# Optimization experiments

Measured on AMD Instinct MI355X. Metric: run time of the kernel, lower is better.

Reference implementation:

```python
import jax, jax.numpy as jnp
import numpy as np

T, H, I, E, TOPK = 4096, 2048, 2048, 16, 2

def setup_inputs() -> dict:
    key = jax.random.key(0)
    k1, k2, k3, k4 = jax.random.split(key, 4)
    return {
        "x": jax.random.normal(k1, (T, H), dtype=jnp.float32),
        "gate_w": jax.random.normal(k2, (E, H), dtype=jnp.float32) * 0.02,
        "ws": jax.random.normal(k3, (E, 2 * I, H), dtype=jnp.float32) * 0.02,
        "w2s": jax.random.normal(k4, (E, H, I), dtype=jnp.float32) * 0.02,
        "top_k": TOPK,
    }

def reference(x, gate_w, ws, w2s, top_k):
    # Router: logits -> softmax -> topk -> renormalize (top_k > 1), per fused_topk.
    logits = x @ gate_w.T                      # [T, E]
    scores = jax.nn.softmax(logits, axis=-1)
    topk_w, topk_ids = jax.lax.top_k(scores, top_k)  # [T, K]
    if top_k > 1:
        topk_w = topk_w / jnp.sum(topk_w, axis=-1, keepdims=True)
    n_exp, two_i, _ = ws.shape
    i_dim = two_i // 2

    def expert_step(acc, inp):
        w13_e, w2_e, e = inp               # [2I,H], [H,I], scalar
        gate_up = x @ w13_e.T              # [T, 2I]
        g, u = gate_up[:, :i_dim], gate_up[:, i_dim:]
        h = jax.nn.silu(g) * u             # SiluAndMul
        y = h @ w2_e.T                     # [T, H]
        coef = jnp.sum(jnp.where(topk_ids == e, topk_w, 0.0), axis=-1)  # [T]
        return acc + coef[:, None] * y, None

    init = jnp.zeros_like(x)
    eids = jnp.arange(n_exp, dtype=topk_ids.dtype)
    out, _ = jax.lax.scan(expert_step, init, (ws, w2s, eids))
    return out
```

## Files before the change

kernel.cpp:

```cpp
#include <hip/hip_runtime.h>
#include <hip/hip_bf16.h>

#define T_DIM 4096
#define H_DIM 2048
#define I_DIM 2048
#define E_NUM 16

#define BM 128
#define BN 128
#define BK 32

#define MAX_ROWS 10240

using frag_ab = __attribute__((ext_vector_type(8))) short;
using frag_cd = __attribute__((ext_vector_type(4))) float;

__device__ __forceinline__ unsigned short f2bf(float f) {
    unsigned int u = __float_as_uint(f);
    u += 0x7fff + ((u >> 16) & 1);
    return (unsigned short)(u >> 16);
}
__device__ __forceinline__ float bf2f(unsigned short s) {
    return __uint_as_float(((unsigned int)s) << 16);
}

__global__ void routing_kernel(const float* __restrict__ x,
                               const float* __restrict__ gw,
                               int* __restrict__ cnt,
                               int* __restrict__ tok_list,
                               float* __restrict__ tok_w) {
    const int wave = threadIdx.x >> 6;
    const int lane = threadIdx.x & 63;
    const int t = blockIdx.x * 4 + wave;
    if (t >= T_DIM) return;

    float acc[E_NUM];
#pragma unroll
    for (int e = 0; e < E_NUM; ++e) acc[e] = 0.f;
    const float* xr = x + (size_t)t * H_DIM;
    for (int j = lane; j < H_DIM; j += 64) {
        float xv = xr[j];
#pragma unroll
        for (int e = 0; e < E_NUM; ++e)
            acc[e] = fmaf(xv, gw[e * H_DIM + j], acc[e]);
    }
#pragma unroll
    for (int e = 0; e < E_NUM; ++e) {
        float v = acc[e];
#pragma unroll
        for (int off = 32; off > 0; off >>= 1) v += __shfl_xor(v, off);
        acc[e] = v;
    }
    if (lane == 0) {
        int b1 = 0; float l1 = acc[0];
#pragma unroll
        for (int e = 1; e < E_NUM; ++e)
            if (acc[e] > l1) { l1 = acc[e]; b1 = e; }
        int b2 = -1; float l2 = -1e30f;
#pragma unroll
        for (int e = 0; e < E_NUM; ++e)
            if (e != b1 && acc[e] > l2) { l2 = acc[e]; b2 = e; }
        float w1 = 1.f / (1.f + __expf(l2 - l1));
        float w2 = 1.f - w1;
        int p1 = atomicAdd(&cnt[b1], 1);
        tok_list[b1 * T_DIM + p1] = t; tok_w[b1 * T_DIM + p1] = w1;
        int p2 = atomicAdd(&cnt[b2], 1);
        tok_list[b2 * T_DIM + p2] = t; tok_w[b2 * T_DIM + p2] = w2;
    }
}

__global__ void scan_kernel(const int* __restrict__ cnt, int* __restrict__ base,
                            int* __restrict__ npad, int* __restrict__ total) {
    int acc = 0;
    for (int e = 0; e < E_NUM; ++e) {
        base[e] = acc;
        int p = (cnt[e] + BM - 1) & ~(BM - 1);
        npad[e] = p;
        acc += p;
    }
    *total = acc;
}

__global__ void __launch_bounds__(256) gemm1_kernel(
    const float* __restrict__ x, const float* __restrict__ ws,
    const int* __restrict__ tok_list,
    const int* __restrict__ cnt, const int* __restrict__ base,
    const int* __restrict__ npad, unsigned short* __restrict__ gu)
{
    const int e = blockIdx.z;
    const int mt = blockIdx.y;
    if (mt * BM >= npad[e]) return;
    const int nt = blockIdx.x;

    __shared__ unsigned short As[BM * BK];
    __shared__ unsigned short Bs[BN * BK];

    const int tid = threadIdx.x;
    const int lane = tid & 63;
    const int wv = tid >> 6;
    const int wm = (wv >> 1) * 64;
    const int wn = (wv & 1) * 64;
    const int quad = lane >> 4;
    const int l16 = lane & 15;

    const int ne = cnt[e];
    const int* tl = tok_list + e * T_DIM + mt * BM;
    const int lim = ne - mt * BM - 1;

    const int ar = tid >> 3;
    const int ac = (tid & 7) * 4;

    const float* xb[4];
#pragma unroll
    for (int it = 0; it < 4; ++it) {
        int r = ar + 32 * it;
        int rr = r < lim ? r : lim;
        xb[it] = x + (size_t)tl[rr] * H_DIM + ac;
    }
    const float* w13 = ws + (size_t)e * (2 * I_DIM) * H_DIM
                          + (size_t)(nt * BN) * H_DIM + ac;

    frag_cd acc[4][4];
#pragma unroll
    for (int i = 0; i < 4; ++i)
#pragma unroll
        for (int j = 0; j < 4; ++j)
            acc[i][j] = (frag_cd){0.f, 0.f, 0.f, 0.f};

    for (int k0 = 0; k0 < H_DIM; k0 += BK) {
#pragma unroll
        for (int it = 0; it < 4; ++it) {
            int r = ar + 32 * it;
            float4 v = *(const float4*)(xb[it] + k0);
            *(ushort4*)(&As[r * BK + ac]) =
                make_ushort4(f2bf(v.x), f2bf(v.y), f2bf(v.z), f2bf(v.w));
            float4 w = *(const float4*)(w13 + (size_t)r * H_DIM + k0);
            *(ushort4*)(&Bs[r * BK + ac]) =
                make_ushort4(f2bf(w.x), f2bf(w.y), f2bf(w.z), f2bf(w.w));
        }
        __syncthreads();
        frag_ab af[4], bf[4];
#pragma unroll
        for (int i = 0; i < 4; ++i) {
            af[i] = *(const frag_ab*)(&As[(wm + i * 16 + l16) * BK + quad * 8]);
            bf[i] = *(const frag_ab*)(&Bs[(wn + i * 16 + l16) * BK + quad * 8]);
        }
#pragma unroll
        for (int i = 0; i < 4; ++i)
#pragma unroll
            for (int j = 0; j < 4; ++j)
                acc[i][j] = __builtin_amdgcn_mfma_f32_16x16x32_bf16(
                    af[i], bf[j], acc[i][j], 0, 0, 0);
        __syncthreads();
    }

    const size_t gbase = (size_t)(base[e] + mt * BM);
#pragma unroll
    for (int i = 0; i < 4; ++i) {
#pragma unroll
        for (int r = 0; r < 4; ++r) {
            int row = wm + i * 16 + quad * 4 + r;
            unsigned short* gr = gu + (gbase + row) * (size_t)(2 * I_DIM) + nt * BN + wn;
#pragma unroll
            for (int j = 0; j < 4; ++j)
                gr[j * 16 + l16] = f2bf(acc[i][j][r]);
        }
    }
}

__global__ void silu_kernel(unsigned short* __restrict__ gu,
                            const int* __restrict__ total) {
    const int tot = *total;
    size_t idx = ((size_t)blockIdx.x * 256 + threadIdx.x) * 4;
    if (idx >= (size_t)tot * I_DIM) return;
    size_t row = idx >> 11;
    int col = (int)(idx & (I_DIM - 1));
    unsigned short* gp = gu + row * (size_t)(2 * I_DIM) + col;
    ushort4 gv = *(const ushort4*)gp;
    ushort4 uv = *(const ushort4*)(gp + I_DIM);
    float g0 = bf2f(gv.x), g1 = bf2f(gv.y), g2 = bf2f(gv.z), g3 = bf2f(gv.w);
    float u0 = bf2f(uv.x), u1 = bf2f(uv.y), u2 = bf2f(uv.z), u3 = bf2f(uv.w);
    float h0 = g0 / (1.f + __expf(-g0)) * u0;
    float h1 = g1 / (1.f + __expf(-g1)) * u1;
    float h2 = g2 / (1.f + __expf(-g2)) * u2;
    float h3 = g3 / (1.f + __expf(-g3)) * u3;
    *(ushort4*)gp = make_ushort4(f2bf(h0), f2bf(h1), f2bf(h2), f2bf(h3));
}

__global__ void __launch_bounds__(256) gemm2_kernel(
    const unsigned short* __restrict__ gu, const float* __restrict__ w2s,
    const int* __restrict__ tok_list, const float* __restrict__ tok_w,
    const int* __restrict__ cnt, const int* __restrict__ base,
    const int* __restrict__ npad, float* __restrict__ out)
{
    const int e = blockIdx.z;
    const int mt = blockIdx.y;
    if (mt * BM >= npad[e]) return;
    const int nt = blockIdx.x;

    __shared__ unsigned short As[BM * BK];
    __shared__ unsigned short Bs[BN * BK];
    __shared__ int s_tok[BM];
    __shared__ float s_tw[BM];

    const int tid = threadIdx.x;
    const int lane = tid & 63;
    const int wv = tid >> 6;
    const int wm = (wv >> 1) * 64;
    const int wn = (wv & 1) * 64;
    const int quad = lane >> 4;
    const int l16 = lane & 15;

    const int ne = cnt[e];
    if (tid < BM) {
        int g = mt * BM + tid;
        bool v = g < ne;
        s_tok[tid] = v ? tok_list[e * T_DIM + g] : -1;
        s_tw[tid]  = v ? tok_w[e * T_DIM + g] : 0.f;
    }

    const size_t abase = (size_t)(base[e] + mt * BM);
    const int ar2 = tid >> 2;
    const int ac2 = (tid & 3) * 8;
    const unsigned short* ab = gu + (abase + ar2) * (size_t)(2 * I_DIM) + ac2;

    const int ar = tid >> 3;
    const int ac = (tid & 7) * 4;
    const float* w2 = w2s + (size_t)e * H_DIM * I_DIM
                          + (size_t)(nt * BN) * I_DIM + ac;

    frag_cd acc[4][4];
#pragma unroll
    for (int i = 0; i < 4; ++i)
#pragma unroll
        for (int j = 0; j < 4; ++j)
            acc[i][j] = (frag_cd){0.f, 0.f, 0.f, 0.f};

    for (int k0 = 0; k0 < I_DIM; k0 += BK) {
        *(uint4*)(&As[ar2 * BK + ac2]) = *(const uint4*)(ab + k0);
        *(uint4*)(&As[(ar2 + 64) * BK + ac2]) =
            *(const uint4*)(ab + (size_t)64 * (2 * I_DIM) + k0);
#pragma unroll
        for (int it = 0; it < 4; ++it) {
            int r = ar + 32 * it;
            float4 w = *(const float4*)(w2 + (size_t)r * I_DIM + k0);
            *(ushort4*)(&Bs[r * BK + ac]) =
                make_ushort4(f2bf(w.x), f2bf(w.y), f2bf(w.z), f2bf(w.w));
        }
        __syncthreads();
        frag_ab af[4], bf[4];
#pragma unroll
        for (int i = 0; i < 4; ++i) {
            af[i] = *(const frag_ab*)(&As[(wm + i * 16 + l16) * BK + quad * 8]);
            bf[i] = *(const frag_ab*)(&Bs[(wn + i * 16 + l16) * BK + quad * 8]);
        }
#pragma unroll
        for (int i = 0; i < 4; ++i)
#pragma unroll
            for (int j = 0; j < 4; ++j)
                acc[i][j] = __builtin_amdgcn_mfma_f32_16x16x32_bf16(
                    af[i], bf[j], acc[i][j], 0, 0, 0);
        __syncthreads();
    }

#pragma unroll
    for (int i = 0; i < 4; ++i) {
#pragma unroll
        for (int r = 0; r < 4; ++r) {
            int row = wm + i * 16 + quad * 4 + r;
            int tok = s_tok[row];
            if (tok < 0) continue;
            float coef = s_tw[row];
            float* orow = out + (size_t)tok * H_DIM + nt * BN + wn;
#pragma unroll
            for (int j = 0; j < 4; ++j)
                atomicAdd(&orow[j * 16 + l16], coef * acc[i][j][r]);
        }
    }
}

extern "C" void kernel_launch(void* const* d_in, const int* in_sizes, int n_in,
                              void* d_out, int out_size, void* d_ws, size_t ws_size,
                              hipStream_t stream) {
    const float* x   = (const float*)d_in[0];
    const float* gw  = (const float*)d_in[1];
    const float* ws  = (const float*)d_in[2];
    const float* w2s = (const float*)d_in[3];

    char* wsp = (char*)d_ws;
    int*   cnt      = (int*)(wsp + 0);
    int*   basep    = (int*)(wsp + 64);
    int*   npad     = (int*)(wsp + 128);
    int*   total    = (int*)(wsp + 192);
    int*   tok_list = (int*)(wsp + 256);
    float* tok_w    = (float*)(wsp + 256 + 4 * E_NUM * T_DIM);
    unsigned short* gu = (unsigned short*)(wsp + 512 + 8 * E_NUM * T_DIM);
    float* out = (float*)d_out;

    hipMemsetAsync(cnt, 0, 64, stream);
    hipMemsetAsync(d_out, 0, (size_t)T_DIM * H_DIM * sizeof(float), stream);

    routing_kernel<<<T_DIM / 4, 256, 0, stream>>>(x, gw, cnt, tok_list, tok_w);
    scan_kernel<<<1, 1, 0, stream>>>(cnt, basep, npad, total);
    gemm1_kernel<<<dim3(2 * I_DIM / BN, T_DIM / BM, E_NUM), 256, 0, stream>>>(
        x, ws, tok_list, cnt, basep, npad, gu);
    silu_kernel<<<(MAX_ROWS * I_DIM / 4) / 256, 256, 0, stream>>>(gu, total);
    gemm2_kernel<<<dim3(H_DIM / BN, T_DIM / BM, E_NUM), 256, 0, stream>>>(
        gu, w2s, tok_list, tok_w, cnt, basep, npad, out);
}
```

Measured before the change: 1.365 ms.

## Pre-convert inputs and weights to bf16 and stage GEMM tiles via direct global-to-LDS loads

Adds a conversion pass that turns x and both expert weight tensors into bf16 buffers in the workspace. New GEMM kernels then load tiles straight into LDS with 16-byte global_load_lds instead of loading fp32, converting in registers and storing to shared memory. This halves the bytes each GEMM tile reads and removes per-iteration conversion ALU work, at the cost of an extra full pass over about 256MB of fp32 weights every call. The fast path runs only when the workspace is at least 482MB; otherwise the old path is kept.

```diff
diff --git a/kernel.cpp b/kernel.cpp
--- a/kernel.cpp
+++ b/kernel.cpp
@@ -14,6 +14,7 @@
 
 using frag_ab = __attribute__((ext_vector_type(8))) short;
 using frag_cd = __attribute__((ext_vector_type(4))) float;
+using ushort8 = __attribute__((ext_vector_type(8))) unsigned short;
 
 __device__ __forceinline__ unsigned short f2bf(float f) {
     unsigned int u = __float_as_uint(f);
@@ -22,6 +23,12 @@
 }
 __device__ __forceinline__ float bf2f(unsigned short s) {
     return __uint_as_float(((unsigned int)s) << 16);
+}
+
+__device__ __forceinline__ void gld16(const void* g, void* l) {
+    __builtin_amdgcn_global_load_lds(
+        (const __attribute__((address_space(1))) unsigned int*)g,
+        (__attribute__((address_space(3))) unsigned int*)l, 16, 0, 0);
 }
 
 __global__ void routing_kernel(const float* __restrict__ x,
@@ -81,8 +88,22 @@
     *total = acc;
 }
 
-__global__ void __launch_bounds__(256) gemm1_kernel(
-    const float* __restrict__ x, const float* __restrict__ ws,
+__global__ void __launch_bounds__(256) cvt_kernel(const float* __restrict__ s,
+                                                  unsigned short* __restrict__ d,
+                                                  size_t n8) {
+    const size_t stride = (size_t)gridDim.x * 256;
+    for (size_t i = (size_t)blockIdx.x * 256 + threadIdx.x; i < n8; i += stride) {
+        const float4* sp = (const float4*)(s + i * 8);
+        float4 a = sp[0], b = sp[1];
+        ushort8 o;
+        o[0] = f2bf(a.x); o[1] = f2bf(a.y); o[2] = f2bf(a.z); o[3] = f2bf(a.w);
+        o[4] = f2bf(b.x); o[5] = f2bf(b.y); o[6] = f2bf(b.z); o[7] = f2bf(b.w);
+        *(ushort8*)(d + i * 8) = o;
+    }
+}
+
+__global__ void __launch_bounds__(256) gemm1_bf_kernel(
+    const unsigned short* __restrict__ xb, const unsigned short* __restrict__ wb,
     const int* __restrict__ tok_list,
     const int* __restrict__ cnt, const int* __restrict__ base,
     const int* __restrict__ npad, unsigned short* __restrict__ gu)
@@ -103,22 +124,24 @@
     const int quad = lane >> 4;
     const int l16 = lane & 15;
 
-    const int ne = cnt[e];
     const int* tl = tok_list + e * T_DIM + mt * BM;
-    const int lim = ne - mt * BM - 1;
-
-    const int ar = tid >> 3;
-    const int ac = (tid & 7) * 4;
-
-    const float* xb[4];
-#pragma unroll
-    for (int it = 0; it < 4; ++it) {
-        int r = ar + 32 * it;
-        int rr = r < lim ? r : lim;
-        xb[it] = x + (size_t)tl[rr] * H_DIM + ac;
-    }
-    const float* w13 = ws + (size_t)e * (2 * I_DIM) * H_DIM
-                          + (size_t)(nt * BN) * H_DIM + ac;
+    const int lim = cnt[e] - mt * BM - 1;
+
+    const int srow = wv * 16 + (lane >> 2);
+    const int scol = (lane & 3) * 8;
+
+    const int r0 = srow      <= lim ? srow      : lim;
+    const int r1 = srow + 64 <= lim ? srow + 64 : lim;
+    const unsigned short* ag0 = xb + (size_t)tl[r0] * H_DIM + scol;
+    const unsigned short* ag1 = xb + (size_t)tl[r1] * H_DIM + scol;
+    const unsigned short* bg0 = wb + (size_t)e * (2 * I_DIM) * H_DIM
+                                   + (size_t)(nt * BN + srow) * H_DIM + scol;
+    const unsigned short* bg1 = bg0 + (size_t)64 * H_DIM;
+
+    unsigned short* al0 = &As[wv * 512];
+    unsigned short* al1 = &As[2048 + wv * 512];
+    unsigned short* bl0 = &Bs[wv * 512];
+    unsigned short* bl1 = &Bs[2048 + wv * 512];
 
     frag_cd acc[4][4];
 #pragma unroll
@@ -128,16 +151,10 @@
             acc[i][j] = (frag_cd){0.f, 0.f, 0.f, 0.f};
 
     for (int k0 = 0; k0 < H_DIM; k0 += BK) {
-#pragma unroll
-        for (int it = 0; it < 4; ++it) {
-            int r = ar + 32 * it;
-            float4 v = *(const float4*)(xb[it] + k0);
-            *(ushort4*)(&As[r * BK + ac]) =
-                make_ushort4(f2bf(v.x), f2bf(v.y), f2bf(v.z), f2bf(v.w));
-            float4 w = *(const float4*)(w13 + (size_t)r * H_DIM + k0);
-            *(ushort4*)(&Bs[r * BK + ac]) =
-                make_ushort4(f2bf(w.x), f2bf(w.y), f2bf(w.z), f2bf(w.w));
-        }
+        gld16(ag0 + k0, al0);
+        gld16(ag1 + k0, al1);
+        gld16(bg0 + k0, bl0);
+        gld16(bg1 + k0, bl1);
         __syncthreads();
         frag_ab af[4], bf[4];
 #pragma unroll
@@ -187,6 +204,184 @@
     *(ushort4*)gp = make_ushort4(f2bf(h0), f2bf(h1), f2bf(h2), f2bf(h3));
 }
 
+__global__ void __launch_bounds__(256) gemm2_bf_kernel(
+    const unsigned short* __restrict__ gu, const unsigned short* __restrict__ w2b,
+    const int* __restrict__ tok_list, const float* __restrict__ tok_w,
+    const int* __restrict__ cnt, const int* __restrict__ base,
+    const int* __restrict__ npad, float* __restrict__ out)
+{
+    const int e = blockIdx.z;
+    const int mt = blockIdx.y;
+    if (mt * BM >= npad[e]) return;
+    const int nt = blockIdx.x;
+
+    __shared__ unsigned short As[BM * BK];
+    __shared__ unsigned short Bs[BN * BK];
+    __shared__ int s_tok[BM];
+    __shared__ float s_tw[BM];
+
+    const int tid = threadIdx.x;
+    const int lane = tid & 63;
+    const int wv = tid >> 6;
+    const int wm = (wv >> 1) * 64;
+    const int wn = (wv & 1) * 64;
+    const int quad = lane >> 4;
+    const int l16 = lane & 15;
+
+    const int ne = cnt[e];
+    if (tid < BM) {
+        int g = mt * BM + tid;
+        bool v = g < ne;
+        s_tok[tid] = v ? tok_list[e * T_DIM + g] : -1;
+        s_tw[tid]  = v ? tok_w[e * T_DIM + g] : 0.f;
+    }
+
+    const size_t abase = (size_t)(base[e] + mt * BM);
+    const int srow = wv * 16 + (lane >> 2);
+    const int scol = (lane & 3) * 8;
+
+    const unsigned short* ag0 = gu + (abase + srow) * (size_t)(2 * I_DIM) + scol;
+    const unsigned short* ag1 = ag0 + (size_t)64 * (2 * I_DIM);
+    const unsigned short* bg0 = w2b + (size_t)e * H_DIM * I_DIM
+                                    + (size_t)(nt * BN + srow) * I_DIM + scol;
+    const unsigned short* bg1 = bg0 + (size_t)64 * I_DIM;
+
+    unsigned short* al0 = &As[wv * 512];
+    unsigned short* al1 = &As[2048 + wv * 512];
+    unsigned short* bl0 = &Bs[wv * 512];
+    unsigned short* bl1 = &Bs[2048 + wv * 512];
+
+    frag_cd acc[4][4];
+#pragma unroll
+    for (int i = 0; i < 4; ++i)
+#pragma unroll
+        for (int j = 0; j < 4; ++j)
+            acc[i][j] = (frag_cd){0.f, 0.f, 0.f, 0.f};
+
+    for (int k0 = 0; k0 < I_DIM; k0 += BK) {
+        gld16(ag0 + k0, al0);
+        gld16(ag1 + k0, al1);
+        gld16(bg0 + k0, bl0);
+        gld16(bg1 + k0, bl1);
+        __syncthreads();
+        frag_ab af[4], bf[4];
+#pragma unroll
+        for (int i = 0; i < 4; ++i) {
+            af[i] = *(const frag_ab*)(&As[(wm + i * 16 + l16) * BK + quad * 8]);
+            bf[i] = *(const frag_ab*)(&Bs[(wn + i * 16 + l16) * BK + quad * 8]);
+        }
+#pragma unroll
+        for (int i = 0; i < 4; ++i)
+#pragma unroll
+            for (int j = 0; j < 4; ++j)
+                acc[i][j] = __builtin_amdgcn_mfma_f32_16x16x32_bf16(
+                    af[i], bf[j], acc[i][j], 0, 0, 0);
+        __syncthreads();
+    }
+
+#pragma unroll
+    for (int i = 0; i < 4; ++i) {
+#pragma unroll
+        for (int r = 0; r < 4; ++r) {
+            int row = wm + i * 16 + quad * 4 + r;
+            int tok = s_tok[row];
+            if (tok < 0) continue;
+            float coef = s_tw[row];
+            float* orow = out + (size_t)tok * H_DIM + nt * BN + wn;
+#pragma unroll
+            for (int j = 0; j < 4; ++j)
+                atomicAdd(&orow[j * 16 + l16], coef * acc[i][j][r]);
+        }
+    }
+}
+
+__global__ void __launch_bounds__(256) gemm1_kernel(
+    const float* __restrict__ x, const float* __restrict__ ws,
+    const int* __restrict__ tok_list,
+    const int* __restrict__ cnt, const int* __restrict__ base,
+    const int* __restrict__ npad, unsigned short* __restrict__ gu)
+{
+    const int e = blockIdx.z;
+    const int mt = blockIdx.y;
+    if (mt * BM >= npad[e]) return;
+    const int nt = blockIdx.x;
+
+    __shared__ unsigned short As[BM * BK];
+    __shared__ unsigned short Bs[BN * BK];
+
+    const int tid = threadIdx.x;
+    const int lane = tid & 63;
+    const int wv = tid >> 6;
+    const int wm = (wv >> 1) * 64;
+    const int wn = (wv & 1) * 64;
+    const int quad = lane >> 4;
+    const int l16 = lane & 15;
+
+    const int ne = cnt[e];
+    const int* tl = tok_list + e * T_DIM + mt * BM;
+    const int lim = ne - mt * BM - 1;
+
+    const int ar = tid >> 3;
+    const int ac = (tid & 7) * 4;
+
+    const float* xb[4];
+#pragma unroll
+    for (int it = 0; it < 4; ++it) {
+        int r = ar + 32 * it;
+        int rr = r < lim ? r : lim;
+        xb[it] = x + (size_t)tl[rr] * H_DIM + ac;
+    }
+    const float* w13 = ws + (size_t)e * (2 * I_DIM) * H_DIM
+                          + (size_t)(nt * BN) * H_DIM + ac;
+
+    frag_cd acc[4][4];
+#pragma unroll
+    for (int i = 0; i < 4; ++i)
+#pragma unroll
+        for (int j = 0; j < 4; ++j)
+            acc[i][j] = (frag_cd){0.f, 0.f, 0.f, 0.f};
+
+    for (int k0 = 0; k0 < H_DIM; k0 += BK) {
+#pragma unroll
+        for (int it = 0; it < 4; ++it) {
+            int r = ar + 32 * it;
+            float4 v = *(const float4*)(xb[it] + k0);
+            *(ushort4*)(&As[r * BK + ac]) =
+                make_ushort4(f2bf(v.x), f2bf(v.y), f2bf(v.z), f2bf(v.w));
+            float4 w = *(const float4*)(w13 + (size_t)r * H_DIM + k0);
+            *(ushort4*)(&Bs[r * BK + ac]) =
+                make_ushort4(f2bf(w.x), f2bf(w.y), f2bf(w.z), f2bf(w.w));
+        }
+        __syncthreads();
+        frag_ab af[4], bf[4];
+#pragma unroll
+        for (int i = 0; i < 4; ++i) {
+            af[i] = *(const frag_ab*)(&As[(wm + i * 16 + l16) * BK + quad * 8]);
+            bf[i] = *(const frag_ab*)(&Bs[(wn + i * 16 + l16) * BK + quad * 8]);
+        }
+#pragma unroll
+        for (int i = 0; i < 4; ++i)
+#pragma unroll
+            for (int j = 0; j < 4; ++j)
+                acc[i][j] = __builtin_amdgcn_mfma_f32_16x16x32_bf16(
+                    af[i], bf[j], acc[i][j], 0, 0, 0);
+        __syncthreads();
+    }
+
+    const size_t gbase = (size_t)(base[e] + mt * BM);
+#pragma unroll
+    for (int i = 0; i < 4; ++i) {
+#pragma unroll
+        for (int r = 0; r < 4; ++r) {
+            int row = wm + i * 16 + quad * 4 + r;
+            unsigned short* gr = gu + (gbase + row) * (size_t)(2 * I_DIM) + nt * BN + wn;
+#pragma unroll
+            for (int j = 0; j < 4; ++j)
+                gr[j * 16 + l16] = f2bf(acc[i][j][r]);
+        }
+    }
+}
+
 __global__ void __launch_bounds__(256) gemm2_kernel(
     const unsigned short* __restrict__ gu, const float* __restrict__ w2s,
     const int* __restrict__ tok_list, const float* __restrict__ tok_w,
@@ -286,25 +481,52 @@
     const float* gw  = (const float*)d_in[1];
     const float* ws  = (const float*)d_in[2];
     const float* w2s = (const float*)d_in[3];
+    float* out = (float*)d_out;
 
     char* wsp = (char*)d_ws;
-    int*   cnt      = (int*)(wsp + 0);
-    int*   basep    = (int*)(wsp + 64);
-    int*   npad     = (int*)(wsp + 128);
-    int*   total    = (int*)(wsp + 192);
-    int*   tok_list = (int*)(wsp + 256);
-    float* tok_w    = (float*)(wsp + 256 + 4 * E_NUM * T_DIM);
-    unsigned short* gu = (unsigned short*)(wsp + 512 + 8 * E_NUM * T_DIM);
-    float* out = (float*)d_out;
+    int* cnt   = (int*)(wsp + 0);
+    int* basep = (int*)(wsp + 64);
+    int* npad  = (int*)(wsp + 128);
+    int* total = (int*)(wsp + 192);
+
+    const size_t MB = (size_t)1 << 20;
+    const size_t NEED = 482 * MB;
 
     hipMemsetAsync(cnt, 0, 64, stream);
     hipMemsetAsync(d_out, 0, (size_t)T_DIM * H_DIM * sizeof(float), stream);
 
-    routing_kernel<<<T_DIM / 4, 256, 0, stream>>>(x, gw, cnt, tok_list, tok_w);
-    scan_kernel<<<1, 1, 0, stream>>>(cnt, basep, npad, total);
-    gemm1_kernel<<<dim3(2 * I_DIM / BN, T_DIM / BM, E_NUM), 256, 0, stream>>>(
-        x, ws, tok_list, cnt, basep, npad, gu);
-    silu_kernel<<<(MAX_ROWS * I_DIM / 4) / 256, 256, 0, stream>>>(gu, total);
-    gemm2_kernel<<<dim3(H_DIM / BN, T_DIM / BM, E_NUM), 256, 0, stream>>>(
-        gu, w2s, tok_list, tok_w, cnt, basep, npad, out);
-}
+    if (ws_size >= NEED) {
+        int*   tok_list = (int*)(wsp + 1 * MB);
+        float* tok_w    = (float*)(wsp + 1 * MB + 512 * 1024);
+        unsigned short* x_bf  = (unsigned short*)(wsp + 2 * MB);
+        unsigned short* gu    = (unsigned short*)(wsp + 18 * MB);
+        unsigned short* ws_bf = (unsigned short*)(wsp + 98 * MB);
+        unsigned short* w2_bf = (unsigned short*)(wsp + 354 * MB);
+
+        cvt_kernel<<<4096, 256, 0, stream>>>(x, x_bf, (size_t)T_DIM * H_DIM / 8);
+        cvt_kernel<<<4096, 256, 0, stream>>>(ws, ws_bf,
+            (size_t)E_NUM * 2 * I_DIM * H_DIM / 8);
+        cvt_kernel<<<4096, 256, 0, stream>>>(w2s, w2_bf,
+            (size_t)E_NUM * H_DIM * I_DIM / 8);
+
+        routing_kernel<<<T_DIM / 4, 256, 0, stream>>>(x, gw, cnt, tok_list, tok_w);
+        scan_kernel<<<1, 1, 0, stream>>>(cnt, basep, npad, total);
+        gemm1_bf_kernel<<<dim3(2 * I_DIM / BN, T_DIM / BM, E_NUM), 256, 0, stream>>>(
+            x_bf, ws_bf, tok_list, cnt, basep, npad, gu);
+        silu_kernel<<<(MAX_ROWS * I_DIM / 4) / 256, 256, 0, stream>>>(gu, total);
+        gemm2_bf_kernel<<<dim3(H_DIM / BN, T_DIM / BM, E_NUM), 256, 0, stream>>>(
+            gu, w2_bf, tok_list, tok_w, cnt, basep, npad, out);
+    } else {
+        int*   tok_list = (int*)(wsp + 256);
+        float* tok_w    = (float*)(wsp + 256 + 4 * E_NUM * T_DIM);
+        unsigned short* gu = (unsigned short*)(wsp + 512 + 8 * E_NUM * T_DIM);
+
+        routing_kernel<<<T_DIM / 4, 256, 0, stream>>>(x, gw, cnt, tok_list, tok_w);
+        scan_kernel<<<1, 1, 0, stream>>>(cnt, basep, npad, total);
+        gemm1_kernel<<<dim3(2 * I_DIM / BN, T_DIM / BM, E_NUM), 256, 0, stream>>>(
+            x, ws, tok_list, cnt, basep, npad, gu);
+        silu_kernel<<<(MAX_ROWS * I_DIM / 4) / 256, 256, 0, stream>>>(gu, total);
+        gemm2_kernel<<<dim3(H_DIM / BN, T_DIM / BM, E_NUM), 256, 0, stream>>>(
+            gu, w2s, tok_list, tok_w, cnt, basep, npad, out);
+    }
+}
```

After: 1.431 ms. 4.8% more time.
